# Optimization experiments

Hardware: AMD Instinct MI355X
Metric: run time of the kernel (lower is better)

The kernel has to match this reference:

```python
import jax, jax.numpy as jnp
import numpy as np

N = 100000  # nodes
E = 1600000  # edges
D = 128     # hid_dim
LN_EPS = 1e-5


def setup_inputs() -> dict:
    key = jax.random.key(0)
    ks = jax.random.split(key, 14)
    s = 1.0 / np.sqrt(D)
    s2 = 1.0 / np.sqrt(2 * D)
    return {
        "x": jax.random.normal(ks[0], (N, D), jnp.float32),
        "ei": jax.random.randint(ks[1], (2, E), 0, N, dtype=jnp.int32),
        # gin1 mlp: Linear(D,D) + LayerNorm(D)
        "W1": jax.random.normal(ks[2], (D, D), jnp.float32) * s,
        "b1": jnp.zeros((D,), jnp.float32),
        "g1": jnp.ones((D,), jnp.float32),
        "bt1": jnp.zeros((D,), jnp.float32),
        # gin2 mlp
        "W2": jax.random.normal(ks[3], (D, D), jnp.float32) * s,
        "b2": jnp.zeros((D,), jnp.float32),
        "g2": jnp.ones((D,), jnp.float32),
        "bt2": jnp.zeros((D,), jnp.float32),
        # merge MLP: Linear(2D,2D) -> ReLU -> Linear(2D,D) -> ReLU
        "Wl1": jax.random.normal(ks[4], (2 * D, 2 * D), jnp.float32) * s2,
        "bl1": jnp.zeros((2 * D,), jnp.float32),
        "Wl2": jax.random.normal(ks[5], (D, 2 * D), jnp.float32) * s2,
        "bl2": jnp.zeros((D,), jnp.float32),
    }


def _layer_norm(h, g, b):
    mu = jnp.mean(h, axis=-1, keepdims=True)
    var = jnp.mean(jnp.square(h - mu), axis=-1, keepdims=True)
    return (h - mu) * jax.lax.rsqrt(var + LN_EPS) * g + b


def _gin_branch(x, src, dst, W, b, g, beta):
    # GINConv with eps=0: h = x + sum_{(src->dst)} x[src]
    agg = jax.ops.segment_sum(x[src], dst, num_segments=N)
    h = x + agg
    # ResBlock(Linear -> LayerNorm -> ReLU)
    y = jax.nn.relu(_layer_norm(h @ W.T + b, g, beta))
    return h + y


def reference(x, ei, W1, b1, g1, bt1, W2, b2, g2, bt2, Wl1, bl1, Wl2, bl2):
    src, dst = ei[0], ei[1]
    ret1 = _gin_branch(x, src, dst, W1, b1, g1, bt1)        # original edges
    ret2 = _gin_branch(x, dst, src, W2, b2, g2, bt2)        # flipped edges ei[[1,0]]
    cat = jnp.concatenate((ret1, ret2), axis=-1)            # [N, 2D]
    h = jax.nn.relu(cat @ Wl1.T + bl1)
    return jax.nn.relu(h @ Wl2.T + bl2)                     # [N, D]
```

## Files before the change

### kernel.cpp

```cpp
#include <hip/hip_runtime.h>
#include <hip/hip_bf16.h>

#define NN 100000
#define EE 1600000
#define DD 128
#define SCAN_N (2 * NN)
#define SCAN_BLOCKS ((SCAN_N + 1023) / 1024)
#define FILL_PASSES 4
#define FILL_RANGE (NN / FILL_PASSES)

typedef unsigned short u16;
typedef __attribute__((ext_vector_type(8))) short short8v;
typedef __attribute__((ext_vector_type(4))) float f32x4;

__device__ inline void bf16split(float v, u16& hi, u16& lo) {
    __hip_bfloat16 h = __float2bfloat16(v);
    hi = *reinterpret_cast<u16*>(&h);
    float r = v - __bfloat162float(h);
    __hip_bfloat16 l = __float2bfloat16(r);
    lo = *reinterpret_cast<u16*>(&l);
}

__global__ __launch_bounds__(256) void k_prep(const float* __restrict__ W1,
                                              const float* __restrict__ W2,
                                              const float* __restrict__ Wl1,
                                              const float* __restrict__ Wl2,
                                              float* __restrict__ Wt1,
                                              float* __restrict__ Wt2,
                                              u16* __restrict__ Wl1hi,
                                              u16* __restrict__ Wl1lo,
                                              u16* __restrict__ Wl2hi,
                                              u16* __restrict__ Wl2lo) {
    int tid = blockIdx.x * 256 + threadIdx.x;
    if (tid < 16384) {
        int r = tid >> 7, c = tid & 127;
        Wt1[c * 128 + r] = W1[tid];
    } else if (tid < 32768) {
        int i = tid - 16384;
        int r = i >> 7, c = i & 127;
        Wt2[c * 128 + r] = W2[i];
    } else if (tid < 98304) {
        int i = tid - 32768;
        bf16split(Wl1[i], Wl1hi[i], Wl1lo[i]);
    } else {
        int i = tid - 98304;
        bf16split(Wl2[i], Wl2hi[i], Wl2lo[i]);
    }
}

__global__ __launch_bounds__(256) void k_count(const int* __restrict__ ei,
                                               int* __restrict__ off) {
    int e = blockIdx.x * 256 + threadIdx.x;
    int s = ei[e];
    int d = ei[EE + e];
    atomicAdd(&off[d], 1);
    atomicAdd(&off[NN + s], 1);
}

__global__ __launch_bounds__(256) void k_scan1(int* __restrict__ off,
                                               int* __restrict__ bsum) {
    __shared__ int s[256];
    int t = threadIdx.x;
    int base = blockIdx.x * 1024 + t * 4;
    int v[4];
    #pragma unroll
    for (int i = 0; i < 4; ++i) {
        int g = base + i;
        v[i] = (g < SCAN_N) ? off[g] : 0;
    }
    int local = v[0] + v[1] + v[2] + v[3];
    s[t] = local;
    __syncthreads();
    #pragma unroll
    for (int o = 1; o < 256; o <<= 1) {
        int add = (t >= o) ? s[t - o] : 0;
        __syncthreads();
        s[t] += add;
        __syncthreads();
    }
    int run = s[t] - local;
    #pragma unroll
    for (int i = 0; i < 4; ++i) {
        int g = base + i;
        if (g < SCAN_N) off[g] = run;
        run += v[i];
    }
    if (t == 0) bsum[blockIdx.x] = s[255];
}

__global__ __launch_bounds__(256) void k_scan2(int* __restrict__ bsum) {
    __shared__ int s[256];
    int t = threadIdx.x;
    int local = (t < SCAN_BLOCKS) ? bsum[t] : 0;
    s[t] = local;
    __syncthreads();
    #pragma unroll
    for (int o = 1; o < 256; o <<= 1) {
        int add = (t >= o) ? s[t - o] : 0;
        __syncthreads();
        s[t] += add;
        __syncthreads();
    }
    if (t < SCAN_BLOCKS) bsum[t] = s[t] - local;
}

__global__ __launch_bounds__(256) void k_scan3(int* __restrict__ off,
                                               const int* __restrict__ bsum,
                                               int* __restrict__ cur) {
    int t = threadIdx.x;
    int base = blockIdx.x * 1024 + t * 4;
    int add = bsum[blockIdx.x];
    #pragma unroll
    for (int i = 0; i < 4; ++i) {
        int g = base + i;
        if (g < SCAN_N) {
            int v = off[g] + add;
            off[g] = v;
            cur[g] = v;
        }
    }
    if (blockIdx.x == 0 && t == 0) off[SCAN_N] = 2 * EE;
}

__global__ __launch_bounds__(256) void k_fill(const int* __restrict__ ei,
                                              int* __restrict__ cur,
                                              int* __restrict__ idx) {
    int b = blockIdx.x;
    int w = b >> 3, myk = b & 7;
    int e = w * 256 + threadIdx.x;
    int s = ei[e];
    int d = ei[EE + e];
    bool ownD = (((d >> 3) & 7) == myk);
    bool ownS = (((s >> 3) & 7) == myk);
    #pragma unroll
    for (int p = 0; p < FILL_PASSES; ++p) {
        if (ownD && d >= p * FILL_RANGE && d < (p + 1) * FILL_RANGE) {
            int p1 = atomicAdd(&cur[d], 1);
            idx[p1] = s;
        }
        if (ownS && s >= p * FILL_RANGE && s < (p + 1) * FILL_RANGE) {
            int p2 = atomicAdd(&cur[NN + s], 1);
            idx[p2] = d;
        }
        __syncthreads();
    }
}

__global__ __launch_bounds__(256) void k_gather(const float4* __restrict__ x4,
                                                const int* __restrict__ off,
                                                const int* __restrict__ idx,
                                                float4* __restrict__ h1,
                                                float4* __restrict__ h2) {
    int t = threadIdx.x;
    int g = blockIdx.x * 8 + (t >> 5);
    int c = t & 31;
    int n = (g < NN) ? g : g - NN;
    int o0 = off[g], o1 = off[g + 1];
    float4 acc = x4[n * 32 + c];
    int j = o0;
    for (; j + 4 <= o1; j += 4) {
        int n0 = idx[j], n1 = idx[j + 1], n2 = idx[j + 2], n3 = idx[j + 3];
        float4 v0 = x4[n0 * 32 + c];
        float4 v1 = x4[n1 * 32 + c];
        float4 v2 = x4[n2 * 32 + c];
        float4 v3 = x4[n3 * 32 + c];
        acc.x += v0.x + v1.x + v2.x + v3.x;
        acc.y += v0.y + v1.y + v2.y + v3.y;
        acc.z += v0.z + v1.z + v2.z + v3.z;
        acc.w += v0.w + v1.w + v2.w + v3.w;
    }
    for (; j < o1; ++j) {
        int nbr = idx[j];
        float4 v = x4[nbr * 32 + c];
        acc.x += v.x; acc.y += v.y; acc.z += v.z; acc.w += v.w;
    }
    float4* hout = (g < NN) ? h1 : h2;
    hout[n * 32 + c] = acc;
}

__global__ __launch_bounds__(256, 4) void k_branch(const float* __restrict__ h1,
                                                   const float* __restrict__ h2,
                                                   const float* __restrict__ Wt1,
                                                   const float* __restrict__ Wt2,
                                                   const float* __restrict__ bias1,
                                                   const float* __restrict__ bias2,
                                                   const float* __restrict__ gam1,
                                                   const float* __restrict__ gam2,
                                                   const float* __restrict__ beta1,
                                                   const float* __restrict__ beta2,
                                                   float* __restrict__ cat) {
    const int br = blockIdx.y;
    const float* h    = br ? h2    : h1;
    const float* Wt   = br ? Wt2   : Wt1;
    const float* bias = br ? bias2 : bias1;
    const float* gam  = br ? gam2  : gam1;
    const float* beta = br ? beta2 : beta1;
    const int colOff  = br ? 128 : 0;

    __shared__ float hsT[32 * 132];
    __shared__ float wst[32 * 132];
    int t = threadIdx.x;
    int m0 = blockIdx.x * 128;
    int my = t >> 4, tx = t & 15, n0 = tx * 8;

    float acc[8][8];
    #pragma unroll
    for (int i = 0; i < 8; ++i)
        #pragma unroll
        for (int j = 0; j < 8; ++j) acc[i][j] = 0.f;

    for (int k0 = 0; k0 < 128; k0 += 32) {
        __syncthreads();
        #pragma unroll
        for (int it = 0; it < 4; ++it) {
            int f = it * 256 + t;
            int row = f >> 3, q = f & 7;
            int node = m0 + row;
            float4 v = make_float4(0.f, 0.f, 0.f, 0.f);
            if (node < NN) v = ((const float4*)h)[node * 32 + (k0 >> 2) + q];
            hsT[(q * 4 + 0) * 132 + row] = v.x;
            hsT[(q * 4 + 1) * 132 + row] = v.y;
            hsT[(q * 4 + 2) * 132 + row] = v.z;
            hsT[(q * 4 + 3) * 132 + row] = v.w;
        }
        #pragma unroll
        for (int it = 0; it < 4; ++it) {
            int f = it * 256 + t;
            int kl = f >> 5, n4 = f & 31;
            *(float4*)&wst[kl * 132 + n4 * 4] = ((const float4*)Wt)[(k0 + kl) * 32 + n4];
        }
        __syncthreads();
        #pragma unroll 4
        for (int kl = 0; kl < 32; ++kl) {
            float4 a0 = *(const float4*)&hsT[kl * 132 + my * 8];
            float4 a1 = *(const float4*)&hsT[kl * 132 + my * 8 + 4];
            float4 b0 = *(const float4*)&wst[kl * 132 + n0];
            float4 b1 = *(const float4*)&wst[kl * 132 + n0 + 4];
            float aa[8] = {a0.x, a0.y, a0.z, a0.w, a1.x, a1.y, a1.z, a1.w};
            float bb[8] = {b0.x, b0.y, b0.z, b0.w, b1.x, b1.y, b1.z, b1.w};
            #pragma unroll
            for (int i = 0; i < 8; ++i)
                #pragma unroll
                for (int j = 0; j < 8; ++j) acc[i][j] += aa[i] * bb[j];
        }
    }

    float breg[8], greg[8], btreg[8];
    #pragma unroll
    for (int j = 0; j < 8; ++j) {
        breg[j]  = bias[n0 + j];
        greg[j]  = gam[n0 + j];
        btreg[j] = beta[n0 + j];
    }
    #pragma unroll
    for (int i = 0; i < 8; ++i) {
        float s = 0.f, q = 0.f;
        #pragma unroll
        for (int j = 0; j < 8; ++j) {
            float v = acc[i][j] + breg[j];
            acc[i][j] = v;
            s += v;
            q += v * v;
        }
        #pragma unroll
        for (int o = 1; o < 16; o <<= 1) {
            s += __shfl_xor(s, o);
            q += __shfl_xor(q, o);
        }
        float mu  = s * (1.f / 128.f);
        float var = q * (1.f / 128.f) - mu * mu;
        float rs  = rsqrtf(var + 1e-5f);
        int node = m0 + my * 8 + i;
        if (node < NN) {
            const float4* hrow = (const float4*)&h[(size_t)node * 128];
            float4 r0 = hrow[tx * 2];
            float4 r1 = hrow[tx * 2 + 1];
            float hres[8] = {r0.x, r0.y, r0.z, r0.w, r1.x, r1.y, r1.z, r1.w};
            float o_[8];
            #pragma unroll
            for (int j = 0; j < 8; ++j) {
                float y = (acc[i][j] - mu) * rs * greg[j] + btreg[j];
                o_[j] = hres[j] + fmaxf(y, 0.f);
            }
            float4* cp = (float4*)&cat[(size_t)node * 256 + colOff + n0];
            cp[0] = make_float4(o_[0], o_[1], o_[2], o_[3]);
            cp[1] = make_float4(o_[4], o_[5], o_[6], o_[7]);
        }
    }
}

__global__ __launch_bounds__(256, 2) void k_mfma_mlp(const float* __restrict__ A,
                                                     const u16* __restrict__ Bhi,
                                                     const u16* __restrict__ Blo,
                                                     const float* __restrict__ bias,
                                                     float* __restrict__ C,
                                                     int ldC) {
    __shared__ u16 ahi[128 * 40], alo[128 * 40], bhi[128 * 40], blo[128 * 40];
    int t = threadIdx.x;
    int m0 = blockIdx.x * 128;
    int nbase = blockIdx.y * 128;
    int lane = t & 63, wid = t >> 6;
    int wm = wid >> 1, wn = wid & 1;
    int lr = lane & 15, lg = lane >> 4;

    f32x4 acc[4][4];
    #pragma unroll
    for (int i = 0; i < 4; ++i)
        #pragma unroll
        for (int j = 0; j < 4; ++j) acc[i][j] = (f32x4){0.f, 0.f, 0.f, 0.f};

    for (int k0 = 0; k0 < 256; k0 += 32) {
        __syncthreads();
        #pragma unroll
        for (int it = 0; it < 4; ++it) {
            int f = it * 256 + t;
            int m = f >> 3, q = f & 7;
            int node = m0 + m;
            float4 v = make_float4(0.f, 0.f, 0.f, 0.f);
            if (node < NN) v = ((const float4*)A)[(size_t)node * 64 + (k0 >> 2) + q];
            u16 h0, l0, h1_, l1_, h2_, l2_, h3, l3;
            bf16split(v.x, h0, l0);
            bf16split(v.y, h1_, l1_);
            bf16split(v.z, h2_, l2_);
            bf16split(v.w, h3, l3);
            uint* ph = (uint*)&ahi[m * 40 + q * 4];
            ph[0] = (uint)h0 | ((uint)h1_ << 16);
            ph[1] = (uint)h2_ | ((uint)h3 << 16);
            uint* pl = (uint*)&alo[m * 40 + q * 4];
            pl[0] = (uint)l0 | ((uint)l1_ << 16);
            pl[1] = (uint)l2_ | ((uint)l3 << 16);
        }
        #pragma unroll
        for (int it = 0; it < 2; ++it) {
            int f = it * 256 + t;
            int n = f >> 2, q = f & 3;
            size_t gsrc = (size_t)(nbase + n) * 256 + k0 + q * 8;
            uint4 vh = *(const uint4*)&Bhi[gsrc];
            uint4 vl = *(const uint4*)&Blo[gsrc];
            *(uint4*)&bhi[n * 40 + q * 8] = vh;
            *(uint4*)&blo[n * 40 + q * 8] = vl;
        }
        __syncthreads();

        short8v afh[4], afl[4];
        #pragma unroll
        for (int mt = 0; mt < 4; ++mt) {
            int r = wm * 64 + mt * 16 + lr;
            afh[mt] = *(const short8v*)&ahi[r * 40 + lg * 8];
            afl[mt] = *(const short8v*)&alo[r * 40 + lg * 8];
        }
        #pragma unroll
        for (int nt = 0; nt < 4; ++nt) {
            int c = wn * 64 + nt * 16 + lr;
            short8v bfh = *(const short8v*)&bhi[c * 40 + lg * 8];
            short8v bfl = *(const short8v*)&blo[c * 40 + lg * 8];
            #pragma unroll
            for (int mt = 0; mt < 4; ++mt) {
                acc[mt][nt] = __builtin_amdgcn_mfma_f32_16x16x32_bf16(afh[mt], bfh, acc[mt][nt], 0, 0, 0);
                acc[mt][nt] = __builtin_amdgcn_mfma_f32_16x16x32_bf16(afh[mt], bfl, acc[mt][nt], 0, 0, 0);
                acc[mt][nt] = __builtin_amdgcn_mfma_f32_16x16x32_bf16(afl[mt], bfh, acc[mt][nt], 0, 0, 0);
            }
        }
    }

    #pragma unroll
    for (int nt = 0; nt < 4; ++nt) {
        int col = nbase + wn * 64 + nt * 16 + lr;
        float bv = bias[col];
        #pragma unroll
        for (int mt = 0; mt < 4; ++mt) {
            #pragma unroll
            for (int r = 0; r < 4; ++r) {
                int row = m0 + wm * 64 + mt * 16 + lg * 4 + r;
                if (row < NN) {
                    float v = fmaxf(acc[mt][nt][r] + bv, 0.f);
                    C[(size_t)row * ldC + col] = v;
                }
            }
        }
    }
}

extern "C" void kernel_launch(void* const* d_in, const int* in_sizes, int n_in,
                              void* d_out, int out_size, void* d_ws, size_t ws_size,
                              hipStream_t stream) {
    const float* x   = (const float*)d_in[0];
    const int*   ei  = (const int*)d_in[1];
    const float* W1  = (const float*)d_in[2];
    const float* b1  = (const float*)d_in[3];
    const float* g1  = (const float*)d_in[4];
    const float* bt1 = (const float*)d_in[5];
    const float* W2  = (const float*)d_in[6];
    const float* b2  = (const float*)d_in[7];
    const float* g2  = (const float*)d_in[8];
    const float* bt2 = (const float*)d_in[9];
    const float* Wl1 = (const float*)d_in[10];
    const float* bl1 = (const float*)d_in[11];
    const float* Wl2 = (const float*)d_in[12];
    const float* bl2 = (const float*)d_in[13];
    float* out = (float*)d_out;

    float* ws    = (float*)d_ws;
    float* h1    = ws;
    float* h2    = ws + (size_t)NN * DD;
    float* mid   = ws;
    float* cat   = ws + (size_t)2 * NN * DD;
    float* Wt1   = ws + (size_t)4 * NN * DD;
    float* Wt2   = Wt1 + 128 * 128;
    u16*   Wl1hi = (u16*)(Wt2 + 128 * 128);
    u16*   Wl1lo = Wl1hi + 256 * 256;
    u16*   Wl2hi = Wl1lo + 256 * 256;
    u16*   Wl2lo = Wl2hi + 128 * 256;
    int*   off   = (int*)(Wl2lo + 128 * 256);
    int*   cur   = off + SCAN_N + 1;
    int*   idx   = cur + SCAN_N;
    int*   bsum  = idx + 2 * EE;

    k_prep<<<512, 256, 0, stream>>>(W1, W2, Wl1, Wl2, Wt1, Wt2,
                                    Wl1hi, Wl1lo, Wl2hi, Wl2lo);

    hipMemsetAsync(off, 0, (SCAN_N + 1) * sizeof(int), stream);
    k_count<<<EE / 256, 256, 0, stream>>>(ei, off);
    k_scan1<<<SCAN_BLOCKS, 256, 0, stream>>>(off, bsum);
    k_scan2<<<1, 256, 0, stream>>>(bsum);
    k_scan3<<<SCAN_BLOCKS, 256, 0, stream>>>(off, bsum, cur);
    k_fill<<<(EE / 256) * 8, 256, 0, stream>>>(ei, cur, idx);

    k_gather<<<SCAN_N / 8, 256, 0, stream>>>((const float4*)x, off, idx,
                                             (float4*)h1, (float4*)h2);

    int nb128 = (NN + 127) / 128;
    k_branch<<<dim3(nb128, 2), 256, 0, stream>>>(h1, h2, Wt1, Wt2,
                                                 b1, b2, g1, g2, bt1, bt2, cat);

    k_mfma_mlp<<<dim3(nb128, 2), 256, 0, stream>>>(cat, Wl1hi, Wl1lo, bl1, mid, 256);
    k_mfma_mlp<<<dim3(nb128, 1), 256, 0, stream>>>(mid, Wl2hi, Wl2lo, bl2, out, 128);
}
```

Baseline: 868.8 us.

## Move branch Linear+LayerNorm GEMM to split-bf16 MFMA and unroll gather by 8

The per-branch 128x128 linear layer now uses bf16 hi/lo split MFMA instructions (three products per tile) instead of an FP32 FMA outer-product loop. Its weights are pre-split in the prep kernel, and the LayerNorm row reduction now goes across two waves through shared memory. The neighbor gather loop is also unrolled to 8 outstanding loads to raise memory-level parallelism. The split-bf16 scheme drops the lo*lo term, so accuracy is slightly below FP32. The epilogue stores are scalar per column rather than float4, which may lower store efficiency.

```diff
diff --git a/kernel.cpp b/kernel.cpp
--- a/kernel.cpp
+++ b/kernel.cpp
@@ -25,20 +25,16 @@
                                               const float* __restrict__ W2,
                                               const float* __restrict__ Wl1,
                                               const float* __restrict__ Wl2,
-                                              float* __restrict__ Wt1,
-                                              float* __restrict__ Wt2,
-                                              u16* __restrict__ Wl1hi,
-                                              u16* __restrict__ Wl1lo,
-                                              u16* __restrict__ Wl2hi,
-                                              u16* __restrict__ Wl2lo) {
+                                              u16* __restrict__ W1hi, u16* __restrict__ W1lo,
+                                              u16* __restrict__ W2hi, u16* __restrict__ W2lo,
+                                              u16* __restrict__ Wl1hi, u16* __restrict__ Wl1lo,
+                                              u16* __restrict__ Wl2hi, u16* __restrict__ Wl2lo) {
     int tid = blockIdx.x * 256 + threadIdx.x;
     if (tid < 16384) {
-        int r = tid >> 7, c = tid & 127;
-        Wt1[c * 128 + r] = W1[tid];
+        bf16split(W1[tid], W1hi[tid], W1lo[tid]);
     } else if (tid < 32768) {
         int i = tid - 16384;
-        int r = i >> 7, c = i & 127;
-        Wt2[c * 128 + r] = W2[i];
+        bf16split(W2[i], W2hi[i], W2lo[i]);
     } else if (tid < 98304) {
         int i = tid - 32768;
         bf16split(Wl1[i], Wl1hi[i], Wl1lo[i]);
@@ -158,133 +154,187 @@
     int o0 = off[g], o1 = off[g + 1];
     float4 acc = x4[n * 32 + c];
     int j = o0;
+    for (; j + 8 <= o1; j += 8) {
+        float4 v0 = x4[idx[j + 0] * 32 + c];
+        float4 v1 = x4[idx[j + 1] * 32 + c];
+        float4 v2 = x4[idx[j + 2] * 32 + c];
+        float4 v3 = x4[idx[j + 3] * 32 + c];
+        float4 v4 = x4[idx[j + 4] * 32 + c];
+        float4 v5 = x4[idx[j + 5] * 32 + c];
+        float4 v6 = x4[idx[j + 6] * 32 + c];
+        float4 v7 = x4[idx[j + 7] * 32 + c];
+        acc.x += v0.x + v1.x + v2.x + v3.x + v4.x + v5.x + v6.x + v7.x;
+        acc.y += v0.y + v1.y + v2.y + v3.y + v4.y + v5.y + v6.y + v7.y;
+        acc.z += v0.z + v1.z + v2.z + v3.z + v4.z + v5.z + v6.z + v7.z;
+        acc.w += v0.w + v1.w + v2.w + v3.w + v4.w + v5.w + v6.w + v7.w;
+    }
     for (; j + 4 <= o1; j += 4) {
-        int n0 = idx[j], n1 = idx[j + 1], n2 = idx[j + 2], n3 = idx[j + 3];
-        float4 v0 = x4[n0 * 32 + c];
-        float4 v1 = x4[n1 * 32 + c];
-        float4 v2 = x4[n2 * 32 + c];
-        float4 v3 = x4[n3 * 32 + c];
+        float4 v0 = x4[idx[j + 0] * 32 + c];
+        float4 v1 = x4[idx[j + 1] * 32 + c];
+        float4 v2 = x4[idx[j + 2] * 32 + c];
+        float4 v3 = x4[idx[j + 3] * 32 + c];
         acc.x += v0.x + v1.x + v2.x + v3.x;
         acc.y += v0.y + v1.y + v2.y + v3.y;
         acc.z += v0.z + v1.z + v2.z + v3.z;
         acc.w += v0.w + v1.w + v2.w + v3.w;
     }
     for (; j < o1; ++j) {
-        int nbr = idx[j];
-        float4 v = x4[nbr * 32 + c];
+        float4 v = x4[idx[j] * 32 + c];
         acc.x += v.x; acc.y += v.y; acc.z += v.z; acc.w += v.w;
     }
     float4* hout = (g < NN) ? h1 : h2;
     hout[n * 32 + c] = acc;
 }
 
-__global__ __launch_bounds__(256, 4) void k_branch(const float* __restrict__ h1,
-                                                   const float* __restrict__ h2,
-                                                   const float* __restrict__ Wt1,
-                                                   const float* __restrict__ Wt2,
-                                                   const float* __restrict__ bias1,
-                                                   const float* __restrict__ bias2,
-                                                   const float* __restrict__ gam1,
-                                                   const float* __restrict__ gam2,
-                                                   const float* __restrict__ beta1,
-                                                   const float* __restrict__ beta2,
-                                                   float* __restrict__ cat) {
+__global__ __launch_bounds__(256, 2) void k_branch_mfma(const float* __restrict__ h1,
+                                                        const float* __restrict__ h2,
+                                                        const u16* __restrict__ W1hi,
+                                                        const u16* __restrict__ W1lo,
+                                                        const u16* __restrict__ W2hi,
+                                                        const u16* __restrict__ W2lo,
+                                                        const float* __restrict__ bias1,
+                                                        const float* __restrict__ bias2,
+                                                        const float* __restrict__ gam1,
+                                                        const float* __restrict__ gam2,
+                                                        const float* __restrict__ beta1,
+                                                        const float* __restrict__ beta2,
+                                                        float* __restrict__ cat) {
     const int br = blockIdx.y;
     const float* h    = br ? h2    : h1;
-    const float* Wt   = br ? Wt2   : Wt1;
+    const u16*  Whi   = br ? W2hi  : W1hi;
+    const u16*  Wlo   = br ? W2lo  : W1lo;
     const float* bias = br ? bias2 : bias1;
     const float* gam  = br ? gam2  : gam1;
     const float* beta = br ? beta2 : beta1;
     const int colOff  = br ? 128 : 0;
 
-    __shared__ float hsT[32 * 132];
-    __shared__ float wst[32 * 132];
+    __shared__ u16 ahi[128 * 40], alo[128 * 40], bhi[128 * 40], blo[128 * 40];
+    __shared__ float red[2][128][2];
     int t = threadIdx.x;
     int m0 = blockIdx.x * 128;
-    int my = t >> 4, tx = t & 15, n0 = tx * 8;
-
-    float acc[8][8];
-    #pragma unroll
-    for (int i = 0; i < 8; ++i)
-        #pragma unroll
-        for (int j = 0; j < 8; ++j) acc[i][j] = 0.f;
+    int lane = t & 63, wid = t >> 6;
+    int wm = wid >> 1, wn = wid & 1;
+    int lr = lane & 15, lg = lane >> 4;
+
+    f32x4 acc[4][4];
+    #pragma unroll
+    for (int i = 0; i < 4; ++i)
+        #pragma unroll
+        for (int j = 0; j < 4; ++j) acc[i][j] = (f32x4){0.f, 0.f, 0.f, 0.f};
 
     for (int k0 = 0; k0 < 128; k0 += 32) {
         __syncthreads();
         #pragma unroll
         for (int it = 0; it < 4; ++it) {
             int f = it * 256 + t;
-            int row = f >> 3, q = f & 7;
+            int m = f >> 3, q = f & 7;
+            int node = m0 + m;
+            float4 v = make_float4(0.f, 0.f, 0.f, 0.f);
+            if (node < NN) v = ((const float4*)h)[(size_t)node * 32 + (k0 >> 2) + q];
+            u16 h0, l0, h1_, l1_, h2_, l2_, h3, l3;
+            bf16split(v.x, h0, l0);
+            bf16split(v.y, h1_, l1_);
+            bf16split(v.z, h2_, l2_);
+            bf16split(v.w, h3, l3);
+            uint* ph = (uint*)&ahi[m * 40 + q * 4];
+            ph[0] = (uint)h0 | ((uint)h1_ << 16);
+            ph[1] = (uint)h2_ | ((uint)h3 << 16);
+            uint* pl = (uint*)&alo[m * 40 + q * 4];
+            pl[0] = (uint)l0 | ((uint)l1_ << 16);
+            pl[1] = (uint)l2_ | ((uint)l3 << 16);
+        }
+        #pragma unroll
+        for (int it = 0; it < 2; ++it) {
+            int f = it * 256 + t;
+            int n = f >> 2, q = f & 3;
+            int gsrc = n * 128 + k0 + q * 8;
+            *(uint4*)&bhi[n * 40 + q * 8] = *(const uint4*)&Whi[gsrc];
+            *(uint4*)&blo[n * 40 + q * 8] = *(const uint4*)&Wlo[gsrc];
+        }
+        __syncthreads();
+
+        short8v afh[4], afl[4];
+        #pragma unroll
+        for (int mt = 0; mt < 4; ++mt) {
+            int r = wm * 64 + mt * 16 + lr;
+            afh[mt] = *(const short8v*)&ahi[r * 40 + lg * 8];
+            afl[mt] = *(const short8v*)&alo[r * 40 + lg * 8];
+        }
+        #pragma unroll
+        for (int nt = 0; nt < 4; ++nt) {
+            int c = wn * 64 + nt * 16 + lr;
+            short8v bfh = *(const short8v*)&bhi[c * 40 + lg * 8];
+            short8v bfl = *(const short8v*)&blo[c * 40 + lg * 8];
+            #pragma unroll
+            for (int mt = 0; mt < 4; ++mt) {
+                acc[mt][nt] = __builtin_amdgcn_mfma_f32_16x16x32_bf16(afh[mt], bfh, acc[mt][nt], 0, 0, 0);
+                acc[mt][nt] = __builtin_amdgcn_mfma_f32_16x16x32_bf16(afh[mt], bfl, acc[mt][nt], 0, 0, 0);
+                acc[mt][nt] = __builtin_amdgcn_mfma_f32_16x16x32_bf16(afl[mt], bfh, acc[mt][nt], 0, 0, 0);
+            }
+        }
+    }
+
+    float breg[4], greg[4], btreg[4];
+    #pragma unroll
+    for (int nt = 0; nt < 4; ++nt) {
+        int col = wn * 64 + nt * 16 + lr;
+        breg[nt]  = bias[col];
+        greg[nt]  = gam[col];
+        btreg[nt] = beta[col];
+    }
+    #pragma unroll
+    for (int mt = 0; mt < 4; ++mt)
+        #pragma unroll
+        for (int nt = 0; nt < 4; ++nt)
+            #pragma unroll
+            for (int r = 0; r < 4; ++r) acc[mt][nt][r] += breg[nt];
+
+    #pragma unroll
+    for (int mt = 0; mt < 4; ++mt) {
+        #pragma unroll
+        for (int r = 0; r < 4; ++r) {
+            float s = 0.f, q = 0.f;
+            #pragma unroll
+            for (int nt = 0; nt < 4; ++nt) {
+                float v = acc[mt][nt][r];
+                s += v;
+                q += v * v;
+            }
+            #pragma unroll
+            for (int o = 1; o < 16; o <<= 1) {
+                s += __shfl_xor(s, o);
+                q += __shfl_xor(q, o);
+            }
+            if (lr == 0) {
+                int row = wm * 64 + mt * 16 + lg * 4 + r;
+                red[wn][row][0] = s;
+                red[wn][row][1] = q;
+            }
+        }
+    }
+    __syncthreads();
+
+    #pragma unroll
+    for (int mt = 0; mt < 4; ++mt) {
+        #pragma unroll
+        for (int r = 0; r < 4; ++r) {
+            int row = wm * 64 + mt * 16 + lg * 4 + r;
             int node = m0 + row;
-            float4 v = make_float4(0.f, 0.f, 0.f, 0.f);
-            if (node < NN) v = ((const float4*)h)[node * 32 + (k0 >> 2) + q];
-            hsT[(q * 4 + 0) * 132 + row] = v.x;
-            hsT[(q * 4 + 1) * 132 + row] = v.y;
-            hsT[(q * 4 + 2) * 132 + row] = v.z;
-            hsT[(q * 4 + 3) * 132 + row] = v.w;
-        }
-        #pragma unroll
-        for (int it = 0; it < 4; ++it) {
-            int f = it * 256 + t;
-            int kl = f >> 5, n4 = f & 31;
-            *(float4*)&wst[kl * 132 + n4 * 4] = ((const float4*)Wt)[(k0 + kl) * 32 + n4];
-        }
-        __syncthreads();
-        #pragma unroll 4
-        for (int kl = 0; kl < 32; ++kl) {
-            float4 a0 = *(const float4*)&hsT[kl * 132 + my * 8];
-            float4 a1 = *(const float4*)&hsT[kl * 132 + my * 8 + 4];
-            float4 b0 = *(const float4*)&wst[kl * 132 + n0];
-            float4 b1 = *(const float4*)&wst[kl * 132 + n0 + 4];
-            float aa[8] = {a0.x, a0.y, a0.z, a0.w, a1.x, a1.y, a1.z, a1.w};
-            float bb[8] = {b0.x, b0.y, b0.z, b0.w, b1.x, b1.y, b1.z, b1.w};
-            #pragma unroll
-            for (int i = 0; i < 8; ++i)
+            float s = red[0][row][0] + red[1][row][0];
+            float q = red[0][row][1] + red[1][row][1];
+            float mu  = s * (1.f / 128.f);
+            float var = q * (1.f / 128.f) - mu * mu;
+            float rs  = rsqrtf(var + 1e-5f);
+            if (node < NN) {
+                const float* hrow = &h[(size_t)node * 128];
                 #pragma unroll
-                for (int j = 0; j < 8; ++j) acc[i][j] += aa[i] * bb[j];
-        }
-    }
-
-    float breg[8], greg[8], btreg[8];
-    #pragma unroll
-    for (int j = 0; j < 8; ++j) {
-        breg[j]  = bias[n0 + j];
-        greg[j]  = gam[n0 + j];
-        btreg[j] = beta[n0 + j];
-    }
-    #pragma unroll
-    for (int i = 0; i < 8; ++i) {
-        float s = 0.f, q = 0.f;
-        #pragma unroll
-        for (int j = 0; j < 8; ++j) {
-            float v = acc[i][j] + breg[j];
-            acc[i][j] = v;
-            s += v;
-            q += v * v;
-        }
-        #pragma unroll
-        for (int o = 1; o < 16; o <<= 1) {
-            s += __shfl_xor(s, o);
-            q += __shfl_xor(q, o);
-        }
-        float mu  = s * (1.f / 128.f);
-        float var = q * (1.f / 128.f) - mu * mu;
-        float rs  = rsqrtf(var + 1e-5f);
-        int node = m0 + my * 8 + i;
-        if (node < NN) {
-            const float4* hrow = (const float4*)&h[(size_t)node * 128];
-            float4 r0 = hrow[tx * 2];
-            float4 r1 = hrow[tx * 2 + 1];
-            float hres[8] = {r0.x, r0.y, r0.z, r0.w, r1.x, r1.y, r1.z, r1.w};
-            float o_[8];
-            #pragma unroll
-            for (int j = 0; j < 8; ++j) {
-                float y = (acc[i][j] - mu) * rs * greg[j] + btreg[j];
-                o_[j] = hres[j] + fmaxf(y, 0.f);
-            }
-            float4* cp = (float4*)&cat[(size_t)node * 256 + colOff + n0];
-            cp[0] = make_float4(o_[0], o_[1], o_[2], o_[3]);
-            cp[1] = make_float4(o_[4], o_[5], o_[6], o_[7]);
+                for (int nt = 0; nt < 4; ++nt) {
+                    int col = wn * 64 + nt * 16 + lr;
+                    float y = (acc[mt][nt][r] - mu) * rs * greg[nt] + btreg[nt];
+                    float o_ = hrow[col] + fmaxf(y, 0.f);
+                    cat[(size_t)node * 256 + colOff + col] = o_;
+                }
+            }
         }
     }
 }
@@ -335,10 +385,8 @@
             int f = it * 256 + t;
             int n = f >> 2, q = f & 3;
             size_t gsrc = (size_t)(nbase + n) * 256 + k0 + q * 8;
-            uint4 vh = *(const uint4*)&Bhi[gsrc];
-            uint4 vl = *(const uint4*)&Blo[gsrc];
-            *(uint4*)&bhi[n * 40 + q * 8] = vh;
-            *(uint4*)&blo[n * 40 + q * 8] = vl;
+            *(uint4*)&bhi[n * 40 + q * 8] = *(const uint4*)&Bhi[gsrc];
+            *(uint4*)&blo[n * 40 + q * 8] = *(const uint4*)&Blo[gsrc];
         }
         __syncthreads();
 
@@ -405,18 +453,21 @@
     float* h2    = ws + (size_t)NN * DD;
     float* mid   = ws;
     float* cat   = ws + (size_t)2 * NN * DD;
-    float* Wt1   = ws + (size_t)4 * NN * DD;
-    float* Wt2   = Wt1 + 128 * 128;
-    u16*   Wl1hi = (u16*)(Wt2 + 128 * 128);
-    u16*   Wl1lo = Wl1hi + 256 * 256;
-    u16*   Wl2hi = Wl1lo + 256 * 256;
-    u16*   Wl2lo = Wl2hi + 128 * 256;
-    int*   off   = (int*)(Wl2lo + 128 * 256);
+    u16*   W1hi  = (u16*)(ws + (size_t)4 * NN * DD);
+    u16*   W1lo  = W1hi + 16384;
+    u16*   W2hi  = W1lo + 16384;
+    u16*   W2lo  = W2hi + 16384;
+    u16*   Wl1hi = W2lo + 16384;
+    u16*   Wl1lo = Wl1hi + 65536;
+    u16*   Wl2hi = Wl1lo + 65536;
+    u16*   Wl2lo = Wl2hi + 32768;
+    int*   off   = (int*)(Wl2lo + 32768);
     int*   cur   = off + SCAN_N + 1;
     int*   idx   = cur + SCAN_N;
     int*   bsum  = idx + 2 * EE;
 
-    k_prep<<<512, 256, 0, stream>>>(W1, W2, Wl1, Wl2, Wt1, Wt2,
+    k_prep<<<512, 256, 0, stream>>>(W1, W2, Wl1, Wl2,
+                                    W1hi, W1lo, W2hi, W2lo,
                                     Wl1hi, Wl1lo, Wl2hi, Wl2lo);
 
     hipMemsetAsync(off, 0, (SCAN_N + 1) * sizeof(int), stream);
@@ -430,8 +481,9 @@
                                              (float4*)h1, (float4*)h2);
 
     int nb128 = (NN + 127) / 128;
-    k_branch<<<dim3(nb128, 2), 256, 0, stream>>>(h1, h2, Wt1, Wt2,
-                                                 b1, b2, g1, g2, bt1, bt2, cat);
+    k_branch_mfma<<<dim3(nb128, 2), 256, 0, stream>>>(h1, h2,
+                                                      W1hi, W1lo, W2hi, W2lo,
+                                                      b1, b2, g1, g2, bt1, bt2, cat);
 
     k_mfma_mlp<<<dim3(nb128, 2), 256, 0, stream>>>(cat, Wl1hi, Wl1lo, bl1, mid, 256);
     k_mfma_mlp<<<dim3(nb128, 1), 256, 0, stream>>>(mid, Wl2hi, Wl2lo, bl2, out, 128);
```

After: 850.1 us. 2.2% less time.
